# Kernel optimization log

Measured on AMD Instinct MI355X. Metric: run time of the kernel, lower is better.

## Reference

```python
import jax, jax.numpy as jnp
import numpy as np

R = 16       # voxel resolution
CH = 64      # channels
NSAMPLE = 16
PROJ = 3


def _bn(x, p, eps):
    # p: [4, C] rows = (gamma, beta, running_mean, running_var); eval-mode BN
    g, b, m, v = p
    sh = [1] * x.ndim
    sh[1] = -1
    return (x - m.reshape(sh)) * (g.reshape(sh) * jax.lax.rsqrt(v.reshape(sh) + eps)) + b.reshape(sh)


def _gather_ch(x, flat_idx):
    # x: [B, C, M], flat_idx: [B, L] -> [B, C, L]
    B, C, _ = x.shape
    idx = jnp.broadcast_to(flat_idx[:, None, :], (B, C, flat_idx.shape[1]))
    return jnp.take_along_axis(x, idx, axis=2)


def _pvb_forward(x, xyz, idx, w3d1, b3d1, bn3d1, w3d2, b3d2, bn3d2, proj_w1, proj_bn, proj_w2, pt_bn):
    B, C, N = x.shape
    r = R
    # ---------- voxelization (coords detached, normalize=False) ----------
    nc = xyz - xyz.mean(axis=2, keepdims=True)
    nc = jnp.clip((nc + 1.0) * 0.5 * r, 0.0, r - 1.0)
    nc = jax.lax.stop_gradient(nc)                        # [B,3,N] float in [0, r-1]
    vi = jnp.round(nc).astype(jnp.int32)
    flat = (vi[:, 0] * r + vi[:, 1]) * r + vi[:, 2]       # [B,N]
    seg = (flat + jnp.arange(B, dtype=jnp.int32)[:, None] * (r ** 3)).reshape(-1)
    feats = x.transpose(0, 2, 1).reshape(B * N, C)
    sums = jax.ops.segment_sum(feats, seg, num_segments=B * r ** 3)
    cnts = jax.ops.segment_sum(jnp.ones((B * N,), x.dtype), seg, num_segments=B * r ** 3)
    v = (sums / jnp.maximum(cnts, 1.0)[:, None]).reshape(B, r, r, r, C).transpose(0, 4, 1, 2, 3)
    # ---------- depthwise Conv3d -> BN3d -> LeakyReLU (x2) ----------
    dn = ('NCDHW', 'OIDHW', 'NCDHW')
    v = jax.lax.conv_general_dilated(v, w3d1, (1, 1, 1), 'SAME', dimension_numbers=dn,
                                     feature_group_count=C) + b3d1.reshape(1, C, 1, 1, 1)
    v = jax.nn.leaky_relu(_bn(v, bn3d1, 1e-4), 0.1)
    v = jax.lax.conv_general_dilated(v, w3d2, (1, 1, 1), 'SAME', dimension_numbers=dn,
                                     feature_group_count=C) + b3d2.reshape(1, C, 1, 1, 1)
    v = jax.nn.leaky_relu(_bn(v, bn3d2, 1e-4), 0.1)
    # ---------- trilinear devoxelize ----------
    vf = v.reshape(B, C, r ** 3)
    lo = jnp.floor(nc).astype(jnp.int32)
    fr = nc - lo
    hi = jnp.minimum(lo + 1, r - 1)
    p_v_x = jnp.zeros((B, C, N), x.dtype)
    for dx in (0, 1):
        for dy in (0, 1):
            for dz in (0, 1):
                xi = hi[:, 0] if dx else lo[:, 0]
                yi = hi[:, 1] if dy else lo[:, 1]
                zi = hi[:, 2] if dz else lo[:, 2]
                w = ((fr[:, 0] if dx else 1.0 - fr[:, 0]) *
                     (fr[:, 1] if dy else 1.0 - fr[:, 1]) *
                     (fr[:, 2] if dz else 1.0 - fr[:, 2]))
                p_v_x = p_v_x + w[:, None, :] * _gather_ch(vf, (xi * r + yi) * r + zi)
    # ---------- neighbor gather (precomputed ball-query idx) ----------
    K = idx.shape[-1]
    flat_nb = idx.reshape(B, N * K)
    x_j = _gather_ch(x, flat_nb).reshape(B, C, N, K)
    xyz_j = _gather_ch(xyz, flat_nb).reshape(B, 3, N, K)
    dp1 = xyz_j - xyz[:, :, :, None]                      # [B,3,N,K]
    df = x_j - x[:, :, :, None]                           # [B,C,N,K]
    # proj_conv: 1x1 conv -> BN2d -> ReLU -> 1x1 conv
    h = jnp.einsum('oc,bcnk->bonk', proj_w1, df)
    h = jax.nn.relu(_bn(h, proj_bn, 1e-5))
    dp2 = jnp.einsum('oc,bcnk->bonk', proj_w2, h)         # [B,3,N,K]
    dp = jnp.concatenate([dp1, dp2], axis=1)              # [B,6,N,K]
    # repeat_interleave of the 6 channels up to C (last gets remainder)
    part = 6
    rep = C // part
    repeats = np.array([rep] * (part - 1) + [C - rep * (part - 1)])
    w = jnp.repeat(dp, repeats, axis=1, total_repeat_length=C)
    x_j = x_j * w
    x_j = jax.nn.relu(_bn(x_j, pt_bn, 1e-5))              # proj_transform
    p_p_x = x_j.max(axis=-1)                              # max-pool over neighbors
    return p_v_x + p_p_x                                  # agg_way == 'add'


def setup_inputs() -> dict:
    key = jax.random.key(0)
    ks = jax.random.split(key, 16)
    B, C, N, K = 4, CH, 16384, NSAMPLE

    def bn_params(k, c):
        k1, k2, k3, k4 = jax.random.split(k, 4)
        return jnp.stack([1.0 + 0.1 * jax.random.normal(k1, (c,), jnp.float32),
                          0.1 * jax.random.normal(k2, (c,), jnp.float32),
                          0.1 * jax.random.normal(k3, (c,), jnp.float32),
                          jax.random.uniform(k4, (c,), jnp.float32, 0.5, 1.5)])

    return dict(
        x=jax.random.normal(ks[0], (B, C, N), jnp.float32),
        xyz=jax.random.uniform(ks[1], (B, 3, N), jnp.float32, -1.0, 1.0),
        idx=jax.random.randint(ks[2], (B, N, K), 0, N, jnp.int32),
        w3d1=0.1 * jax.random.normal(ks[3], (C, 1, 3, 3, 3), jnp.float32),
        b3d1=0.01 * jax.random.normal(ks[4], (C,), jnp.float32),
        bn3d1=bn_params(ks[5], C),
        w3d2=0.1 * jax.random.normal(ks[6], (C, 1, 3, 3, 3), jnp.float32),
        b3d2=0.01 * jax.random.normal(ks[7], (C,), jnp.float32),
        bn3d2=bn_params(ks[8], C),
        proj_w1=0.1 * jax.random.normal(ks[9], (PROJ, C), jnp.float32),
        proj_bn=bn_params(ks[10], PROJ),
        proj_w2=0.3 * jax.random.normal(ks[11], (PROJ, PROJ), jnp.float32),
        pt_bn=bn_params(ks[12], C),
    )


def reference(x, xyz, idx, w3d1, b3d1, bn3d1, w3d2, b3d2, bn3d2, proj_w1, proj_bn, proj_w2, pt_bn):
    return _pvb_forward(x, xyz, idx, w3d1, b3d1, bn3d1, w3d2, b3d2, bn3d2, proj_w1, proj_bn, proj_w2, pt_bn)
```

## Files before the change

### kernel.cpp

```cpp
#include <hip/hip_runtime.h>

namespace {
constexpr int B_  = 4;
constexpr int C_  = 64;
constexpr int N_  = 16384;
constexpr int K_  = 16;
constexpr int R3_ = 4096;

constexpr int OFF_MEANS = 0;
constexpr int OFF_XT    = 16;
constexpr int OFF_PTS   = OFF_XT  + B_*N_*C_/2;
constexpr int OFF_SUMS  = OFF_PTS + B_*N_*8;
constexpr int OFF_CNTS  = OFF_SUMS + B_*R3_*C_;
constexpr int OFF_VT    = OFF_CNTS + B_*R3_;
constexpr int OFF_VOX2  = OFF_VT   + B_*C_*R3_;
constexpr int FILL_FLOATS = B_*R3_*C_ + B_*R3_;
constexpr int FILL_BLOCKS = FILL_FLOATS / (256 * 4);
}

__device__ __forceinline__ unsigned short f2bf(float f) {
  unsigned u = __float_as_uint(f);
  return (unsigned short)((u + 0x7FFFu + ((u >> 16) & 1u)) >> 16);
}
__device__ __forceinline__ unsigned cvtpk_bf16(float lo, float hi) {
  unsigned r;
  asm("v_cvt_pk_bf16_f32 %0, %1, %2" : "=v"(r) : "v"(lo), "v"(hi));
  return r;
}

__global__ __launch_bounds__(256) void k_init(
    const float* __restrict__ xyz, float* __restrict__ means,
    float* __restrict__ fill) {
  const int blk = blockIdx.x;
  if (blk >= 12) {
    const int base = (blk - 12) * (256 * 4) + threadIdx.x * 4;
    *(float4*)(fill + base) = make_float4(0.f, 0.f, 0.f, 0.f);
    return;
  }
  __shared__ double red[256];
  const float* p = xyz + blk * N_;
  double s = 0.0;
  for (int i = threadIdx.x; i < N_; i += 256) s += (double)p[i];
  red[threadIdx.x] = s;
  __syncthreads();
  for (int st = 128; st; st >>= 1) {
    if (threadIdx.x < st) red[threadIdx.x] += red[threadIdx.x + st];
    __syncthreads();
  }
  if (threadIdx.x == 0) means[blk] = (float)(red[0] * (1.0 / (double)N_));
}

__global__ __launch_bounds__(256) void k_prep(
    const float* __restrict__ x, const float* __restrict__ xyz,
    const float* __restrict__ pw1, const float* __restrict__ means,
    unsigned short* __restrict__ xT, float* __restrict__ pts,
    float* __restrict__ sums, float* __restrict__ cnts) {
  __shared__ float tile[64 * 65];
  __shared__ float ncs[3][64];
  __shared__ int   flats[64];

  const int t   = threadIdx.x;
  const int blk = blockIdx.x;
  const int b   = blk >> 8;
  const int n0  = (blk & 255) << 6;

#pragma unroll
  for (int i = 0; i < 4; ++i) {
    int c = i * 16 + (t >> 4);
    int j4 = (t & 15) * 4;
    float4 v = *(const float4*)&x[((size_t)(b * C_ + c)) * N_ + n0 + j4];
    tile[c * 65 + j4 + 0] = v.x;
    tile[c * 65 + j4 + 1] = v.y;
    tile[c * 65 + j4 + 2] = v.z;
    tile[c * 65 + j4 + 3] = v.w;
  }
  __syncthreads();

  unsigned* __restrict__ xT32 = (unsigned*)xT;
#pragma unroll
  for (int i = 0; i < 8; ++i) {
    int p = i * 8 + (t >> 5);
    int c2 = (t & 31) * 2;
    unsigned pk = cvtpk_bf16(tile[c2 * 65 + p], tile[(c2 + 1) * 65 + p]);
    xT32[((size_t)(b * N_ + n0 + p)) * 32 + (t & 31)] = pk;
  }

  if (t < 192) {
    int p = t & 63, q = t >> 6;
    float s = 0.f;
#pragma unroll
    for (int c = 0; c < 64; ++c) s = fmaf(pw1[q * 64 + c], tile[c * 65 + p], s);
    size_t pb = ((size_t)(b * N_ + n0 + p)) * 8;
    pts[pb + 3 + q] = s;
    float v = xyz[((size_t)(b * 3 + q)) * N_ + n0 + p];
    pts[pb + q] = v;
    float nc = fminf(fmaxf((v - means[b * 3 + q] + 1.0f) * 8.0f, 0.0f), 15.0f);
    ncs[q][p] = nc;
  } else {
    int p = t & 63;
    size_t pb = ((size_t)(b * N_ + n0 + p)) * 8;
    pts[pb + 6] = 0.f;
    pts[pb + 7] = 0.f;
  }
  __syncthreads();

  if (t < 64) {
    int vx = (int)rintf(ncs[0][t]);
    int vy = (int)rintf(ncs[1][t]);
    int vz = (int)rintf(ncs[2][t]);
    int f = (vx * 16 + vy) * 16 + vz;
    flats[t] = f;
    atomicAdd(&cnts[b * R3_ + f], 1.0f);
  }
  __syncthreads();

  const int w = t >> 6, lane = t & 63;
#pragma unroll
  for (int i = 0; i < 16; ++i) {
    int p = w * 16 + i;
    int f = flats[p];
    atomicAdd(&sums[((size_t)(b * R3_ + f)) * C_ + lane], tile[lane * 65 + p]);
  }
}

__global__ __launch_bounds__(256) void k_tr(
    const float* __restrict__ sums, const float* __restrict__ cnts,
    float* __restrict__ vT) {
  __shared__ float tile[64 * 65];
  const int t = threadIdx.x;
  const int b = blockIdx.x >> 6;
  const int v0 = (blockIdx.x & 63) << 6;

#pragma unroll
  for (int i = 0; i < 16; ++i) {
    int r = i * 4 + (t >> 6);
    int c = t & 63;
    tile[r * 65 + c] = sums[((size_t)(b * R3_ + v0 + r)) * C_ + c];
  }
  const float rcnt = 1.0f / fmaxf(cnts[b * R3_ + v0 + (t & 63)], 1.0f);
  __syncthreads();
#pragma unroll
  for (int i = 0; i < 16; ++i) {
    int c = i * 4 + (t >> 6);
    int r = t & 63;
    vT[((size_t)(b * C_ + c)) * R3_ + v0 + r] = tile[r * 65 + c] * rcnt;
  }
}

__global__ __launch_bounds__(256) void k_conv(
    const float* __restrict__ vT,
    const float* __restrict__ w3d1, const float* __restrict__ b3d1,
    const float* __restrict__ bn1, const float* __restrict__ w3d2,
    const float* __restrict__ b3d2, const float* __restrict__ bn2,
    unsigned short* __restrict__ vox2) {
  __shared__ float va[18 * 18 * 18];
  __shared__ float vb[18 * 18 * 18];
  const int t = threadIdx.x;
  const int b = blockIdx.x >> 6;
  const int c = blockIdx.x & 63;

  float W1[27], W2[27];
#pragma unroll
  for (int i = 0; i < 27; ++i) { W1[i] = w3d1[c * 27 + i]; W2[i] = w3d2[c * 27 + i]; }
  const float s1 = bn1[c] / sqrtf(bn1[192 + c] + 1e-4f);
  const float d1 = (b3d1[c] - bn1[128 + c]) * s1 + bn1[64 + c];
  const float s2 = bn2[c] / sqrtf(bn2[192 + c] + 1e-4f);
  const float d2 = (b3d2[c] - bn2[128 + c]) * s2 + bn2[64 + c];

  for (int i = t; i < 18 * 18 * 18; i += 256) { va[i] = 0.f; vb[i] = 0.f; }
  const float* __restrict__ vrow = vT + ((size_t)(b * C_ + c)) * R3_;
  __syncthreads();

#pragma unroll
  for (int i = 0; i < 16; ++i) {
    int vox = t + i * 256;
    int z = vox & 15, y = (vox >> 4) & 15, xx = vox >> 8;
    va[((xx + 1) * 18 + (y + 1)) * 18 + (z + 1)] = vrow[vox];
  }
  __syncthreads();

#pragma unroll
  for (int i = 0; i < 16; ++i) {
    int vox = t + i * 256;
    int z = vox & 15, y = (vox >> 4) & 15, xx = vox >> 8;
    int base = ((xx + 1) * 18 + (y + 1)) * 18 + (z + 1);
    float acc = 0.f;
#pragma unroll
    for (int dx = -1; dx <= 1; ++dx)
#pragma unroll
      for (int dy = -1; dy <= 1; ++dy)
#pragma unroll
        for (int dz = -1; dz <= 1; ++dz)
          acc = fmaf(W1[((dx + 1) * 3 + (dy + 1)) * 3 + (dz + 1)],
                     va[base + dx * 324 + dy * 18 + dz], acc);
    float tt = acc * s1 + d1;
    vb[base] = tt > 0.f ? tt : 0.1f * tt;
  }
  __syncthreads();

#pragma unroll
  for (int i = 0; i < 16; ++i) {
    int vox = t + i * 256;
    int z = vox & 15, y = (vox >> 4) & 15, xx = vox >> 8;
    int base = ((xx + 1) * 18 + (y + 1)) * 18 + (z + 1);
    float acc = 0.f;
#pragma unroll
    for (int dx = -1; dx <= 1; ++dx)
#pragma unroll
      for (int dy = -1; dy <= 1; ++dy)
#pragma unroll
        for (int dz = -1; dz <= 1; ++dz)
          acc = fmaf(W2[((dx + 1) * 3 + (dy + 1)) * 3 + (dz + 1)],
                     vb[base + dx * 324 + dy * 18 + dz], acc);
    float tt = acc * s2 + d2;
    vox2[((size_t)(b * R3_ + vox)) * C_ + c] = f2bf(tt > 0.f ? tt : 0.1f * tt);
  }
}

__global__ __launch_bounds__(256, 8) void k_final(
    const unsigned short* __restrict__ xT, const float* __restrict__ pts,
    const unsigned short* __restrict__ vox2, const int* __restrict__ idx,
    const float* __restrict__ means, const float* __restrict__ pbn,
    const float* __restrict__ pw2, const float* __restrict__ ptbn,
    float* __restrict__ out) {
  __shared__ unsigned w6[3][513];
  __shared__ int      jarr[512];
  __shared__ unsigned dv[32][8];
  __shared__ float    outT[64 * 33];

  const int t = threadIdx.x;
  const int blk = blockIdx.x;
  const int xcd = blk & 7;
  const int b = xcd >> 1;
  const int t32 = ((blk >> 3) << 1) | (xcd & 1);
  const int n0 = t32 * 32;

  const float psc0 = pbn[0] * rsqrtf(pbn[9]  + 1e-5f);
  const float psc1 = pbn[1] * rsqrtf(pbn[10] + 1e-5f);
  const float psc2 = pbn[2] * rsqrtf(pbn[11] + 1e-5f);
  const float pof0 = pbn[3] - pbn[6] * psc0;
  const float pof1 = pbn[4] - pbn[7] * psc1;
  const float pof2 = pbn[5] - pbn[8] * psc2;
  float W2r[9];
#pragma unroll
  for (int i = 0; i < 9; ++i) W2r[i] = pw2[i];

  const float* __restrict__ ptsb = pts + (size_t)b * N_ * 8;

#pragma unroll
  for (int rep = 0; rep < 2; ++rep) {
    const int q = t + rep * 256;
    const int p = q >> 4;
    const int n = n0 + p;
    const int j = idx[(size_t)b * N_ * K_ + (size_t)n0 * K_ + q];
    jarr[q] = j;
    const float* qr = ptsb + (size_t)j * 8;
    float4 qa = *(const float4*)qr;
    float4 qb = *(const float4*)(qr + 4);
    const float* ir = ptsb + (size_t)n * 8;
    float4 pa = *(const float4*)ir;
    float4 pb = *(const float4*)(ir + 4);
    float d0 = qa.x - pa.x, d1 = qa.y - pa.y, d2 = qa.z - pa.z;
    float c0 = pof0 - psc0 * pa.w;
    float c1 = pof1 - psc1 * pb.x;
    float c2 = pof2 - psc2 * pb.y;
    float h0 = fmaxf(fmaf(qa.w, psc0, c0), 0.f);
    float h1 = fmaxf(fmaf(qb.x, psc1, c1), 0.f);
    float h2 = fmaxf(fmaf(qb.y, psc2, c2), 0.f);
    float e0 = fmaf(W2r[0], h0, fmaf(W2r[1], h1, W2r[2] * h2));
    float e1 = fmaf(W2r[3], h0, fmaf(W2r[4], h1, W2r[5] * h2));
    float e2 = fmaf(W2r[6], h0, fmaf(W2r[7], h1, W2r[8] * h2));
    w6[0][q] = cvtpk_bf16(d0, d1);
    w6[1][q] = cvtpk_bf16(d2, e0);
    w6[2][q] = cvtpk_bf16(e1, e2);
  }

  if (t < 32) {
    const int n = n0 + t;
    const float* ir = ptsb + (size_t)n * 8;
    float x0 = ir[0], x1 = ir[1], x2 = ir[2];
    float nc0 = fminf(fmaxf((x0 - means[b * 3 + 0] + 1.0f) * 8.0f, 0.0f), 15.0f);
    float nc1 = fminf(fmaxf((x1 - means[b * 3 + 1] + 1.0f) * 8.0f, 0.0f), 15.0f);
    float nc2 = fminf(fmaxf((x2 - means[b * 3 + 2] + 1.0f) * 8.0f, 0.0f), 15.0f);
    int lx = (int)nc0, ly = (int)nc1, lz = (int)nc2;
    float fx = nc0 - (float)lx, fy = nc1 - (float)ly, fz = nc2 - (float)lz;
    int hx = lx < 15 ? lx + 1 : 15;
    int hy = ly < 15 ? ly + 1 : 15;
    int hz = lz < 15 ? lz + 1 : 15;
    float wx[2] = {1.f - fx, fx};
    float wy[2] = {1.f - fy, fy};
    float wz[2] = {1.f - fz, fz};
    int xi[2] = {lx, hx}, yi[2] = {ly, hy}, zi[2] = {lz, hz};
#pragma unroll
    for (int c8 = 0; c8 < 8; ++c8) {
      int dx = c8 >> 2, dy = (c8 >> 1) & 1, dz = c8 & 1;
      int flat = (xi[dx] * 16 + yi[dy]) * 16 + zi[dz];
      float wt = wx[dx] * wy[dy] * wz[dz];
      dv[t][c8] = ((unsigned)flat << 16) | (unsigned)f2bf(wt);
    }
  }
  __syncthreads();

  const int w = t >> 6, lane = t & 63;
  const unsigned voff = (unsigned)lane * 2u;
  const int widx = lane < 20 ? 0 : lane < 40 ? 1 : 2;
  const bool hi = (lane >= 10 && lane < 20) || (lane >= 30 && lane < 40) || (lane >= 50);
  const unsigned shl = hi ? 0u : 16u;
  const float ts = ptbn[lane] * rsqrtf(ptbn[192 + lane] + 1e-5f);
  const float td = ptbn[64 + lane] - ptbn[128 + lane] * ts;
  const unsigned short* __restrict__ xTb = xT + (size_t)b * N_ * C_;
  const unsigned short* __restrict__ voxb = vox2 + (size_t)b * R3_ * C_;

  float g[24];
#pragma unroll
  for (int z = 0; z < 24; ++z) g[z] = 0.f;

#pragma unroll
  for (int i = 0; i < 8; ++i) {
    const int p = i * 4 + w;
    const int pq = p * 16;

    unsigned dvu[8];
#pragma unroll
    for (int c8 = 0; c8 < 8; ++c8) {
      dvu[c8] = (unsigned)__builtin_amdgcn_readfirstlane((int)dv[p][c8]);
      const unsigned short* bp = voxb + ((size_t)(dvu[c8] >> 16) << 6);
      asm volatile("global_load_short_d16_hi %0, %1, %2"
                   : "+v"(g[c8]) : "v"(voff), "s"(bp));
    }
#pragma unroll
    for (int k = 0; k < 16; ++k) {
      int jb = __builtin_amdgcn_readfirstlane(jarr[pq + k]);
      const unsigned short* bp = xTb + ((size_t)jb << 6);
      asm volatile("global_load_short_d16_hi %0, %1, %2"
                   : "+v"(g[8 + k]) : "v"(voff), "s"(bp));
    }
    asm volatile("s_waitcnt vmcnt(0)" ::: "memory");
    __builtin_amdgcn_sched_barrier(0);

    float acc = 0.f;
#pragma unroll
    for (int c8 = 0; c8 < 8; ++c8)
      acc = fmaf(__uint_as_float(dvu[c8] << 16), g[c8], acc);

    float pm = 0.f;
#pragma unroll
    for (int k = 0; k < 16; ++k) {
      float wf = __uint_as_float(w6[widx][pq + k] << shl);
      pm = fmaxf(pm, fmaf(g[8 + k] * wf, ts, td));
    }

    outT[lane * 33 + p] = acc + pm;
  }
  __syncthreads();

#pragma unroll
  for (int i = 0; i < 8; ++i) {
    int c = i * 8 + (t >> 5);
    int col = t & 31;
    out[((size_t)(b * C_ + c)) * N_ + n0 + col] = outT[c * 33 + col];
  }
}

extern "C" void kernel_launch(void* const* d_in, const int* in_sizes, int n_in,
                              void* d_out, int out_size, void* d_ws, size_t ws_size,
                              hipStream_t stream) {
  const float* x     = (const float*)d_in[0];
  const float* xyz   = (const float*)d_in[1];
  const int*   idx   = (const int*)  d_in[2];
  const float* w3d1  = (const float*)d_in[3];
  const float* b3d1  = (const float*)d_in[4];
  const float* bn3d1 = (const float*)d_in[5];
  const float* w3d2  = (const float*)d_in[6];
  const float* b3d2  = (const float*)d_in[7];
  const float* bn3d2 = (const float*)d_in[8];
  const float* pw1   = (const float*)d_in[9];
  const float* pbn   = (const float*)d_in[10];
  const float* pw2   = (const float*)d_in[11];
  const float* ptbn  = (const float*)d_in[12];
  float* out = (float*)d_out;
  float* ws  = (float*)d_ws;

  k_init<<<dim3(12 + FILL_BLOCKS), dim3(256), 0, stream>>>(
      xyz, ws + OFF_MEANS, ws + OFF_SUMS);
  k_prep<<<dim3(B_ * N_ / 64), dim3(256), 0, stream>>>(
      x, xyz, pw1, ws + OFF_MEANS, (unsigned short*)(ws + OFF_XT), ws + OFF_PTS,
      ws + OFF_SUMS, ws + OFF_CNTS);
  k_tr<<<dim3(B_ * 64), dim3(256), 0, stream>>>(
      ws + OFF_SUMS, ws + OFF_CNTS, ws + OFF_VT);
  k_conv<<<dim3(B_ * C_), dim3(256), 0, stream>>>(
      ws + OFF_VT, w3d1, b3d1, bn3d1, w3d2, b3d2, bn3d2,
      (unsigned short*)(ws + OFF_VOX2));
  k_final<<<dim3(B_ * N_ / 32), dim3(256), 0, stream>>>(
      (const unsigned short*)(ws + OFF_XT), ws + OFF_PTS,
      (const unsigned short*)(ws + OFF_VOX2), idx, ws + OFF_MEANS,
      pbn, pw2, ptbn, out);
}
```

Measured before the change: 90.33 us.

## Use bf16 voxel and neighbor-point buffers; register-blocked z-row depthwise conv

Three changes. k_tr now writes the normalized voxel grid as packed bf16 instead of fp32, which halves that intermediate buffer. k_prep writes a compact 16-byte bf16 copy of each point's xyz and projection values, so the random neighbor gather in k_final reads one uint4 instead of two float4s. k_conv is restructured so each thread computes a full 16-voxel z-row in registers from float4 shared-memory row loads, using padded rows of 20. This cuts shared-memory loads per output, at the cost of extra bf16 rounding error in the voxel values and neighbor coordinates.

```diff
diff --git a/kernel.cpp b/kernel.cpp
--- a/kernel.cpp
+++ b/kernel.cpp
@@ -9,11 +9,12 @@
 
 constexpr int OFF_MEANS = 0;
 constexpr int OFF_XT    = 16;
-constexpr int OFF_PTS   = OFF_XT  + B_*N_*C_/2;
-constexpr int OFF_SUMS  = OFF_PTS + B_*N_*8;
+constexpr int OFF_PTS   = OFF_XT   + B_*N_*C_/2;
+constexpr int OFF_PTSH  = OFF_PTS  + B_*N_*8;
+constexpr int OFF_SUMS  = OFF_PTSH + B_*N_*4;
 constexpr int OFF_CNTS  = OFF_SUMS + B_*R3_*C_;
-constexpr int OFF_VT    = OFF_CNTS + B_*R3_;
-constexpr int OFF_VOX2  = OFF_VT   + B_*C_*R3_;
+constexpr int OFF_VT16  = OFF_CNTS + B_*R3_;
+constexpr int OFF_VOX2  = OFF_VT16 + B_*C_*R3_/2;
 constexpr int FILL_FLOATS = B_*R3_*C_ + B_*R3_;
 constexpr int FILL_BLOCKS = FILL_FLOATS / (256 * 4);
 }
@@ -27,6 +28,8 @@
   asm("v_cvt_pk_bf16_f32 %0, %1, %2" : "=v"(r) : "v"(lo), "v"(hi));
   return r;
 }
+__device__ __forceinline__ float bflo(unsigned u) { return __uint_as_float(u << 16); }
+__device__ __forceinline__ float bfhi(unsigned u) { return __uint_as_float(u & 0xffff0000u); }
 
 __global__ __launch_bounds__(256) void k_init(
     const float* __restrict__ xyz, float* __restrict__ means,
@@ -54,9 +57,12 @@
     const float* __restrict__ x, const float* __restrict__ xyz,
     const float* __restrict__ pw1, const float* __restrict__ means,
     unsigned short* __restrict__ xT, float* __restrict__ pts,
+    unsigned* __restrict__ ptsh,
     float* __restrict__ sums, float* __restrict__ cnts) {
   __shared__ float tile[64 * 65];
   __shared__ float ncs[3][64];
+  __shared__ float xys[3][64];
+  __shared__ float hps[3][64];
   __shared__ int   flats[64];
 
   const int t   = threadIdx.x;
@@ -92,8 +98,10 @@
     for (int c = 0; c < 64; ++c) s = fmaf(pw1[q * 64 + c], tile[c * 65 + p], s);
     size_t pb = ((size_t)(b * N_ + n0 + p)) * 8;
     pts[pb + 3 + q] = s;
+    hps[q][p] = s;
     float v = xyz[((size_t)(b * 3 + q)) * N_ + n0 + p];
     pts[pb + q] = v;
+    xys[q][p] = v;
     float nc = fminf(fmaxf((v - means[b * 3 + q] + 1.0f) * 8.0f, 0.0f), 15.0f);
     ncs[q][p] = nc;
   } else {
@@ -111,6 +119,12 @@
     int f = (vx * 16 + vy) * 16 + vz;
     flats[t] = f;
     atomicAdd(&cnts[b * R3_ + f], 1.0f);
+    uint4 r;
+    r.x = cvtpk_bf16(xys[0][t], xys[1][t]);
+    r.y = cvtpk_bf16(xys[2][t], hps[0][t]);
+    r.z = cvtpk_bf16(hps[1][t], hps[2][t]);
+    r.w = 0u;
+    *(uint4*)&ptsh[((size_t)(b * N_ + n0 + t)) * 4] = r;
   }
   __syncthreads();
 
@@ -125,8 +139,9 @@
 
 __global__ __launch_bounds__(256) void k_tr(
     const float* __restrict__ sums, const float* __restrict__ cnts,
-    float* __restrict__ vT) {
+    unsigned* __restrict__ vT16) {
   __shared__ float tile[64 * 65];
+  __shared__ float rs[64];
   const int t = threadIdx.x;
   const int b = blockIdx.x >> 6;
   const int v0 = (blockIdx.x & 63) << 6;
@@ -137,24 +152,27 @@
     int c = t & 63;
     tile[r * 65 + c] = sums[((size_t)(b * R3_ + v0 + r)) * C_ + c];
   }
-  const float rcnt = 1.0f / fmaxf(cnts[b * R3_ + v0 + (t & 63)], 1.0f);
-  __syncthreads();
-#pragma unroll
-  for (int i = 0; i < 16; ++i) {
-    int c = i * 4 + (t >> 6);
-    int r = t & 63;
-    vT[((size_t)(b * C_ + c)) * R3_ + v0 + r] = tile[r * 65 + c] * rcnt;
+  if (t < 64) rs[t] = 1.0f / fmaxf(cnts[b * R3_ + v0 + t], 1.0f);
+  __syncthreads();
+
+#pragma unroll
+  for (int i = 0; i < 8; ++i) {
+    int d = t + i * 256;
+    int c = d >> 5, vp = (d & 31) * 2;
+    unsigned pk = cvtpk_bf16(tile[vp * 65 + c] * rs[vp],
+                             tile[(vp + 1) * 65 + c] * rs[vp + 1]);
+    vT16[((size_t)(b * C_ + c)) * 2048 + (v0 >> 1) + (d & 31)] = pk;
   }
 }
 
 __global__ __launch_bounds__(256) void k_conv(
-    const float* __restrict__ vT,
+    const unsigned* __restrict__ vT16,
     const float* __restrict__ w3d1, const float* __restrict__ b3d1,
     const float* __restrict__ bn1, const float* __restrict__ w3d2,
     const float* __restrict__ b3d2, const float* __restrict__ bn2,
     unsigned short* __restrict__ vox2) {
-  __shared__ float va[18 * 18 * 18];
-  __shared__ float vb[18 * 18 * 18];
+  __shared__ float va[18 * 18 * 20];
+  __shared__ float vb[18 * 18 * 20];
   const int t = threadIdx.x;
   const int b = blockIdx.x >> 6;
   const int c = blockIdx.x & 63;
@@ -167,58 +185,88 @@
   const float s2 = bn2[c] / sqrtf(bn2[192 + c] + 1e-4f);
   const float d2 = (b3d2[c] - bn2[128 + c]) * s2 + bn2[64 + c];
 
-  for (int i = t; i < 18 * 18 * 18; i += 256) { va[i] = 0.f; vb[i] = 0.f; }
-  const float* __restrict__ vrow = vT + ((size_t)(b * C_ + c)) * R3_;
-  __syncthreads();
-
-#pragma unroll
-  for (int i = 0; i < 16; ++i) {
-    int vox = t + i * 256;
-    int z = vox & 15, y = (vox >> 4) & 15, xx = vox >> 8;
-    va[((xx + 1) * 18 + (y + 1)) * 18 + (z + 1)] = vrow[vox];
-  }
-  __syncthreads();
-
-#pragma unroll
-  for (int i = 0; i < 16; ++i) {
-    int vox = t + i * 256;
-    int z = vox & 15, y = (vox >> 4) & 15, xx = vox >> 8;
-    int base = ((xx + 1) * 18 + (y + 1)) * 18 + (z + 1);
-    float acc = 0.f;
-#pragma unroll
-    for (int dx = -1; dx <= 1; ++dx)
-#pragma unroll
-      for (int dy = -1; dy <= 1; ++dy)
-#pragma unroll
-        for (int dz = -1; dz <= 1; ++dz)
-          acc = fmaf(W1[((dx + 1) * 3 + (dy + 1)) * 3 + (dz + 1)],
-                     va[base + dx * 324 + dy * 18 + dz], acc);
-    float tt = acc * s1 + d1;
-    vb[base] = tt > 0.f ? tt : 0.1f * tt;
-  }
-  __syncthreads();
-
-#pragma unroll
-  for (int i = 0; i < 16; ++i) {
-    int vox = t + i * 256;
-    int z = vox & 15, y = (vox >> 4) & 15, xx = vox >> 8;
-    int base = ((xx + 1) * 18 + (y + 1)) * 18 + (z + 1);
-    float acc = 0.f;
-#pragma unroll
-    for (int dx = -1; dx <= 1; ++dx)
-#pragma unroll
-      for (int dy = -1; dy <= 1; ++dy)
-#pragma unroll
-        for (int dz = -1; dz <= 1; ++dz)
-          acc = fmaf(W2[((dx + 1) * 3 + (dy + 1)) * 3 + (dz + 1)],
-                     vb[base + dx * 324 + dy * 18 + dz], acc);
-    float tt = acc * s2 + d2;
-    vox2[((size_t)(b * R3_ + vox)) * C_ + c] = f2bf(tt > 0.f ? tt : 0.1f * tt);
+  for (int i = t; i < 18 * 18 * 20; i += 256) { va[i] = 0.f; vb[i] = 0.f; }
+  const unsigned* __restrict__ vrow = vT16 + ((size_t)(b * C_ + c)) * 2048;
+  __syncthreads();
+
+#pragma unroll
+  for (int i = 0; i < 8; ++i) {
+    int d = t + i * 256;
+    unsigned u = vrow[d];
+    int vox0 = d * 2;
+    int z = vox0 & 15, y = (vox0 >> 4) & 15, xx = vox0 >> 8;
+    int base = ((xx + 1) * 18 + (y + 1)) * 20 + (z + 1);
+    va[base]     = bflo(u);
+    va[base + 1] = bfhi(u);
+  }
+  __syncthreads();
+
+  const int x = t >> 4, y = t & 15;
+  float acc[16];
+
+#pragma unroll
+  for (int z = 0; z < 16; ++z) acc[z] = 0.f;
+#pragma unroll
+  for (int dx = 0; dx < 3; ++dx)
+#pragma unroll
+    for (int dy = 0; dy < 3; ++dy) {
+      const float* row = &va[((x + dx) * 18 + (y + dy)) * 20];
+      float wv[18];
+      *(float4*)&wv[0]  = *(const float4*)&row[0];
+      *(float4*)&wv[4]  = *(const float4*)&row[4];
+      *(float4*)&wv[8]  = *(const float4*)&row[8];
+      *(float4*)&wv[12] = *(const float4*)&row[12];
+      wv[16] = row[16]; wv[17] = row[17];
+      const float k0 = W1[(dx * 3 + dy) * 3 + 0];
+      const float k1 = W1[(dx * 3 + dy) * 3 + 1];
+      const float k2 = W1[(dx * 3 + dy) * 3 + 2];
+#pragma unroll
+      for (int z = 0; z < 16; ++z)
+        acc[z] = fmaf(k0, wv[z], fmaf(k1, wv[z + 1], fmaf(k2, wv[z + 2], acc[z])));
+    }
+  {
+    const int wb = ((x + 1) * 18 + (y + 1)) * 20 + 1;
+#pragma unroll
+    for (int z = 0; z < 16; ++z) {
+      float tt = acc[z] * s1 + d1;
+      vb[wb + z] = tt > 0.f ? tt : 0.1f * tt;
+    }
+  }
+  __syncthreads();
+
+#pragma unroll
+  for (int z = 0; z < 16; ++z) acc[z] = 0.f;
+#pragma unroll
+  for (int dx = 0; dx < 3; ++dx)
+#pragma unroll
+    for (int dy = 0; dy < 3; ++dy) {
+      const float* row = &vb[((x + dx) * 18 + (y + dy)) * 20];
+      float wv[18];
+      *(float4*)&wv[0]  = *(const float4*)&row[0];
+      *(float4*)&wv[4]  = *(const float4*)&row[4];
+      *(float4*)&wv[8]  = *(const float4*)&row[8];
+      *(float4*)&wv[12] = *(const float4*)&row[12];
+      wv[16] = row[16]; wv[17] = row[17];
+      const float k0 = W2[(dx * 3 + dy) * 3 + 0];
+      const float k1 = W2[(dx * 3 + dy) * 3 + 1];
+      const float k2 = W2[(dx * 3 + dy) * 3 + 2];
+#pragma unroll
+      for (int z = 0; z < 16; ++z)
+        acc[z] = fmaf(k0, wv[z], fmaf(k1, wv[z + 1], fmaf(k2, wv[z + 2], acc[z])));
+    }
+  {
+    const int vbase = (x * 16 + y) * 16;
+#pragma unroll
+    for (int z = 0; z < 16; ++z) {
+      float tt = acc[z] * s2 + d2;
+      vox2[((size_t)(b * R3_ + vbase + z)) * C_ + c] = f2bf(tt > 0.f ? tt : 0.1f * tt);
+    }
   }
 }
 
 __global__ __launch_bounds__(256, 8) void k_final(
     const unsigned short* __restrict__ xT, const float* __restrict__ pts,
+    const unsigned* __restrict__ ptsh,
     const unsigned short* __restrict__ vox2, const int* __restrict__ idx,
     const float* __restrict__ means, const float* __restrict__ pbn,
     const float* __restrict__ pw2, const float* __restrict__ ptbn,
@@ -246,6 +294,7 @@
   for (int i = 0; i < 9; ++i) W2r[i] = pw2[i];
 
   const float* __restrict__ ptsb = pts + (size_t)b * N_ * 8;
+  const unsigned* __restrict__ ptshb = ptsh + (size_t)b * N_ * 4;
 
 #pragma unroll
   for (int rep = 0; rep < 2; ++rep) {
@@ -254,19 +303,20 @@
     const int n = n0 + p;
     const int j = idx[(size_t)b * N_ * K_ + (size_t)n0 * K_ + q];
     jarr[q] = j;
-    const float* qr = ptsb + (size_t)j * 8;
-    float4 qa = *(const float4*)qr;
-    float4 qb = *(const float4*)(qr + 4);
+    uint4 q4 = *(const uint4*)(ptshb + (size_t)j * 4);
+    const float qx0 = bflo(q4.x), qx1 = bfhi(q4.x);
+    const float qx2 = bflo(q4.y), qh0 = bfhi(q4.y);
+    const float qh1 = bflo(q4.z), qh2 = bfhi(q4.z);
     const float* ir = ptsb + (size_t)n * 8;
     float4 pa = *(const float4*)ir;
     float4 pb = *(const float4*)(ir + 4);
-    float d0 = qa.x - pa.x, d1 = qa.y - pa.y, d2 = qa.z - pa.z;
+    float d0 = qx0 - pa.x, d1 = qx1 - pa.y, d2 = qx2 - pa.z;
     float c0 = pof0 - psc0 * pa.w;
     float c1 = pof1 - psc1 * pb.x;
     float c2 = pof2 - psc2 * pb.y;
-    float h0 = fmaxf(fmaf(qa.w, psc0, c0), 0.f);
-    float h1 = fmaxf(fmaf(qb.x, psc1, c1), 0.f);
-    float h2 = fmaxf(fmaf(qb.y, psc2, c2), 0.f);
+    float h0 = fmaxf(fmaf(qh0, psc0, c0), 0.f);
+    float h1 = fmaxf(fmaf(qh1, psc1, c1), 0.f);
+    float h2 = fmaxf(fmaf(qh2, psc2, c2), 0.f);
     float e0 = fmaf(W2r[0], h0, fmaf(W2r[1], h1, W2r[2] * h2));
     float e1 = fmaf(W2r[3], h0, fmaf(W2r[4], h1, W2r[5] * h2));
     float e2 = fmaf(W2r[6], h0, fmaf(W2r[7], h1, W2r[8] * h2));
@@ -385,14 +435,15 @@
       xyz, ws + OFF_MEANS, ws + OFF_SUMS);
   k_prep<<<dim3(B_ * N_ / 64), dim3(256), 0, stream>>>(
       x, xyz, pw1, ws + OFF_MEANS, (unsigned short*)(ws + OFF_XT), ws + OFF_PTS,
-      ws + OFF_SUMS, ws + OFF_CNTS);
+      (unsigned*)(ws + OFF_PTSH), ws + OFF_SUMS, ws + OFF_CNTS);
   k_tr<<<dim3(B_ * 64), dim3(256), 0, stream>>>(
-      ws + OFF_SUMS, ws + OFF_CNTS, ws + OFF_VT);
+      ws + OFF_SUMS, ws + OFF_CNTS, (unsigned*)(ws + OFF_VT16));
   k_conv<<<dim3(B_ * C_), dim3(256), 0, stream>>>(
-      ws + OFF_VT, w3d1, b3d1, bn3d1, w3d2, b3d2, bn3d2,
+      (const unsigned*)(ws + OFF_VT16), w3d1, b3d1, bn3d1, w3d2, b3d2, bn3d2,
       (unsigned short*)(ws + OFF_VOX2));
   k_final<<<dim3(B_ * N_ / 32), dim3(256), 0, stream>>>(
       (const unsigned short*)(ws + OFF_XT), ws + OFF_PTS,
+      (const unsigned*)(ws + OFF_PTSH),
       (const unsigned short*)(ws + OFF_VOX2), idx, ws + OFF_MEANS,
       pbn, pw2, ptbn, out);
 }
```

Measured after the change: 90.66 us. About the same (+0.4%).
